# Optimization experiments

Hardware: AMD Instinct MI355X
Metric: run time of the kernel (lower is better)

The kernel has to match this reference:

```python
import jax, jax.numpy as jnp
import numpy as np

K = 3  # three_nn
EPS = 1e-10


def setup_inputs() -> dict:
    key = jax.random.key(0)
    ks = jax.random.split(key, 10)
    B, N, NP = 4, 16384, 4096
    C1, C2 = 128, 256
    Cin, H1, H2, Cout = C1 + C2, 256, 256, 128
    xyz1 = jax.random.normal(ks[0], (B, N, 3), dtype=jnp.float32)
    xyz2 = jax.random.normal(ks[1], (B, NP, 3), dtype=jnp.float32)
    features1 = jax.random.normal(ks[2], (B, N, C1), dtype=jnp.float32)
    features2 = jax.random.normal(ks[3], (B, NP, C2), dtype=jnp.float32)
    def lin(k, fan_in, fan_out):
        bound = 1.0 / np.sqrt(fan_in)
        kw, kb = jax.random.split(k)
        W = jax.random.uniform(kw, (fan_in, fan_out), jnp.float32, -bound, bound)
        b = jax.random.uniform(kb, (fan_out,), jnp.float32, -bound, bound)
        return W, b
    W1, b1 = lin(ks[4], Cin, H1)
    W2, b2 = lin(ks[5], H1, H2)
    W3, b3 = lin(ks[6], H2, Cout)
    return {"xyz1": xyz1, "xyz2": xyz2, "features1": features1,
            "features2": features2, "W1": W1, "b1": b1, "W2": W2,
            "b2": b2, "W3": W3, "b3": b3}


def _three_nn(xyz1, xyz2):
    # squared pairwise distances via |a|^2 + |b|^2 - 2 a.b  -> [B, N, npoint]
    sq1 = jnp.sum(xyz1 * xyz1, axis=-1)  # [B, N]
    sq2 = jnp.sum(xyz2 * xyz2, axis=-1)  # [B, npoint]
    dots = jnp.einsum("bnd,bmd->bnm", xyz1, xyz2)
    sqdist = sq1[:, :, None] + sq2[:, None, :] - 2.0 * dots
    neg_d, idx = jax.lax.top_k(-sqdist, K)  # 3 smallest squared distances
    return -neg_d, idx  # dist:[B,N,3], idx:[B,N,3]


def reference(xyz1, xyz2, features1, features2, W1, b1, W2, b2, W3, b3):
    B = xyz1.shape[0]
    dist, idx = _three_nn(xyz1, xyz2)
    # torch custom three_nn is non-differentiable in dist
    dist = jax.lax.stop_gradient(dist)
    dist = jnp.maximum(dist, EPS)
    recip = 1.0 / dist                                  # [B, N, 3]
    weight = recip / jnp.sum(recip, axis=-1, keepdims=True)
    # three_interpolate: gather neighbor features and weighted-sum
    batch_idx = jnp.arange(B)[:, None, None]
    gathered = features2[batch_idx, idx]                # [B, N, 3, C2]
    interp = jnp.einsum("bnkc,bnk->bnc", gathered, weight)
    new_features = jnp.concatenate([features1, interp], axis=-1)
    h = jax.nn.relu(new_features @ W1 + b1)
    h = jax.nn.relu(h @ W2 + b2)
    return h @ W3 + b3
```

## Files before the change

kernel.cpp:

```cpp
#include <hip/hip_runtime.h>
#include <stdint.h>

#define QT   65536
#define NPTS 4096
#define C1   128
#define C2   256
#define CIN  384
#define COUT 128

typedef _Float16 f16;
typedef __attribute__((ext_vector_type(8))) _Float16 f16x8;
typedef __attribute__((ext_vector_type(4))) float f32x4;

__device__ __attribute__((aligned(16))) f16 g_w1p[12 * 16 * 64 * 8];
__device__ __attribute__((aligned(16))) f16 g_w2p[8 * 16 * 64 * 8];
__device__ __attribute__((aligned(16))) f16 g_w3p[8 * 8 * 64 * 8];
__device__ __attribute__((aligned(16))) float4 g_cand[4 * NPTS];

__device__ inline void packW4(const float* __restrict__ W, f16* __restrict__ dst,
                              int i, int N, int NCB) {
  const int g = i & 3, quad = (i >> 2) & 3, cbk = i >> 4;
  const int cb = cbk % NCB, kcb = cbk / NCB;
  const int col = cb * 16 + g * 4;
  const int k0 = kcb * 32 + quad * 8;
  f16x8 o[4];
#pragma unroll
  for (int e = 0; e < 8; ++e) {
    float4 v = *(const float4*)(W + (size_t)(k0 + e) * N + col);
    o[0][e] = (f16)v.x; o[1][e] = (f16)v.y; o[2][e] = (f16)v.z; o[3][e] = (f16)v.w;
  }
  f16* base = dst + ((size_t)cbk * 64 + quad * 16 + g * 4) * 8;
#pragma unroll
  for (int j = 0; j < 4; ++j) *(f16x8*)(base + j * 8) = o[j];
}

__global__ __launch_bounds__(256) void prep(
    const float* __restrict__ xyz2, const float* __restrict__ W1,
    const float* __restrict__ W2,   const float* __restrict__ W3) {
  const int tid = blockIdx.x * 256 + threadIdx.x;
  const int nthr = gridDim.x * 256;
  for (int i = tid; i < 4 * NPTS; i += nthr) {
    const float* p = xyz2 + (size_t)i * 3;
    float x = p[0], y = p[1], z = p[2];
    g_cand[i] = make_float4(x, y, z, fmaf(x, x, fmaf(y, y, z * z)));
  }
  for (int i = tid; i < 12 * 16 * 16; i += nthr) packW4(W1, g_w1p, i, 256, 16);
  for (int i = tid; i < 8 * 16 * 16; i += nthr) packW4(W2, g_w2p, i, 256, 16);
  for (int i = tid; i < 8 * 8 * 16; i += nthr) packW4(W3, g_w3p, i, 128, 8);
}

__device__ inline uint32_t umin(uint32_t a, uint32_t b) { return a < b ? a : b; }
__device__ inline uint32_t med3u(uint32_t a, uint32_t b, uint32_t c) {
  uint32_t d;
  asm("v_med3_u32 %0, %1, %2, %3" : "=v"(d) : "v"(a), "v"(b), "v"(c));
  return d;
}

#define XS_STRIDE 392
#define HS_STRIDE 264
#define WV_OFF 50176
#define IV_OFF 51200
#define SMEM_BYTES 52224

__global__ __launch_bounds__(512) void fused_fp(
    const float* __restrict__ xyz1, const float* __restrict__ xyz2,
    const float* __restrict__ f1,   const float* __restrict__ f2,
    const float* __restrict__ W1,   const float* __restrict__ b1,
    const float* __restrict__ W2,   const float* __restrict__ b2,
    const float* __restrict__ W3,   const float* __restrict__ b3,
    float* __restrict__ out)
{
  __shared__ __align__(16) char smem[SMEM_BYTES];
  uint32_t* mgU  = (uint32_t*)(smem + 16384);
  float*    wvp  = (float*)(smem + WV_OFF);
  int*      ivp  = (int*)(smem + IV_OFF);
  f16*      Xs   = (f16*)smem;
  f16*      Hs   = (f16*)smem;

  const int t = threadIdx.x;
  const int r = t & 63;
  const int w = t >> 6;
  const int qb = blockIdx.x * 64;
  const int batch = qb >> 14;
  const float* xz2b = xyz2 + (size_t)batch * NPTS * 3;
  const float* f2b  = f2   + (size_t)batch * NPTS * C2;

  const int q = qb + r;
  const float qx = xyz1[q * 3], qy = xyz1[q * 3 + 1], qz = xyz1[q * 3 + 2];
  const float nx = -2.f * qx, ny = -2.f * qy, nz = -2.f * qz;
  const float sq1q = qx * qx + qy * qy + qz * qz;

  uint32_t k0 = ~0u, k1 = ~0u, k2 = ~0u, k3 = ~0u, k4 = ~0u;

  auto ins5 = [&](uint32_t c) {
    uint32_t n0 = umin(k0, c);
    uint32_t n1 = med3u(k0, k1, c);
    uint32_t n2 = med3u(k1, k2, c);
    uint32_t n3 = med3u(k2, k3, c);
    uint32_t n4 = med3u(k3, k4, c);
    k0 = n0; k1 = n1; k2 = n2; k3 = n3; k4 = n4;
  };
  auto packk = [&](float e, uint32_t idx) -> uint32_t {
    e = fmaxf(e, 0.f);
    return (__builtin_bit_cast(uint32_t, e) & 0xFFFFF000u) | idx;
  };

  {
    const int wu = __builtin_amdgcn_readfirstlane(w);
    const float4* __restrict__ cp = g_cand + (batch << 12) + (wu << 9);
    const uint32_t abase = (uint32_t)(wu << 9);
    #pragma unroll 2
    for (int m = 0; m < 512; m += 4) {
      float4 c0 = cp[m], c1 = cp[m + 1], c2 = cp[m + 2], c3 = cp[m + 3];
      float e0 = fmaf(nx, c0.x, fmaf(ny, c0.y, fmaf(nz, c0.z, c0.w))) + sq1q;
      float e1 = fmaf(nx, c1.x, fmaf(ny, c1.y, fmaf(nz, c1.z, c1.w))) + sq1q;
      float e2 = fmaf(nx, c2.x, fmaf(ny, c2.y, fmaf(nz, c2.z, c2.w))) + sq1q;
      float e3 = fmaf(nx, c3.x, fmaf(ny, c3.y, fmaf(nz, c3.z, c3.w))) + sq1q;
      ins5(packk(e0, abase + m));
      ins5(packk(e1, abase + m + 1));
      ins5(packk(e2, abase + m + 2));
      ins5(packk(e3, abase + m + 3));
    }
  }

  if (w > 0) {
    int base = ((w - 1) * 64 + r) * 5;
    mgU[base]     = k0;
    mgU[base + 1] = k1;
    mgU[base + 2] = k2;
    mgU[base + 3] = k3;
    mgU[base + 4] = k4;
  }
  __syncthreads();

  if (w == 0) {
    const double x1 = (double)qx, y1 = (double)qy, z1 = (double)qz;
    const double sq1 = x1 * x1 + y1 * y1 + z1 * z1;
    double d0 = 1e300, d1 = 1e300, d2 = 1e300;
    int j0 = 0, j1 = 0, j2 = 0;
    uint32_t surv[40];
    surv[0] = k0; surv[1] = k1; surv[2] = k2; surv[3] = k3; surv[4] = k4;
    #pragma unroll
    for (int wi = 0; wi < 7; ++wi)
      #pragma unroll
      for (int s = 0; s < 5; ++s)
        surv[5 + wi * 5 + s] = mgU[(wi * 64 + r) * 5 + s];
    #pragma unroll
    for (int s = 0; s < 40; ++s) {
      int idx = (int)(surv[s] & (NPTS - 1));
      const float* p2 = xz2b + (size_t)idx * 3;
      double x2 = (double)p2[0], y2 = (double)p2[1], z2 = (double)p2[2];
      double d = sq1 + (x2 * x2 + y2 * y2 + z2 * z2)
                     - 2.0 * (x1 * x2 + y1 * y2 + z1 * z2);
      bool c2 = (d < d2) || (d == d2 && idx < j2);
      bool c1 = (d < d1) || (d == d1 && idx < j1);
      bool c0 = (d < d0) || (d == d0 && idx < j0);
      d2 = c1 ? d1 : (c2 ? d : d2);  j2 = c1 ? j1 : (c2 ? idx : j2);
      d1 = c0 ? d0 : (c1 ? d : d1);  j1 = c0 ? j0 : (c1 ? idx : j1);
      d0 = c0 ? d : d0;              j0 = c0 ? idx : j0;
    }
    float e0 = fmaxf((float)d0, 1e-10f);
    float e1 = fmaxf((float)d1, 1e-10f);
    float e2 = fmaxf((float)d2, 1e-10f);
    float r0 = 1.f / e0, r1 = 1.f / e1, r2 = 1.f / e2;
    float inv = 1.f / (r0 + r1 + r2);
    wvp[r * 4 + 0] = r0 * inv; wvp[r * 4 + 1] = r1 * inv;
    wvp[r * 4 + 2] = r2 * inv; wvp[r * 4 + 3] = 0.f;
    ivp[r * 4 + 0] = j0; ivp[r * 4 + 1] = j1; ivp[r * 4 + 2] = j2; ivp[r * 4 + 3] = 0;
  }
  __syncthreads();

  {
    const int row = t >> 3, c = t & 7;
    f16* xr = Xs + row * XS_STRIDE;
    {
      const float* f1r = f1 + (size_t)(qb + row) * C1 + c * 16;
      float4 u0 = *(const float4*)(f1r);
      float4 u1 = *(const float4*)(f1r + 4);
      float4 u2 = *(const float4*)(f1r + 8);
      float4 u3 = *(const float4*)(f1r + 12);
      f16x8 o0, o1;
      o0[0] = (f16)u0.x; o0[1] = (f16)u0.y; o0[2] = (f16)u0.z; o0[3] = (f16)u0.w;
      o0[4] = (f16)u1.x; o0[5] = (f16)u1.y; o0[6] = (f16)u1.z; o0[7] = (f16)u1.w;
      o1[0] = (f16)u2.x; o1[1] = (f16)u2.y; o1[2] = (f16)u2.z; o1[3] = (f16)u2.w;
      o1[4] = (f16)u3.x; o1[5] = (f16)u3.y; o1[6] = (f16)u3.z; o1[7] = (f16)u3.w;
      *(f16x8*)(xr + c * 16)     = o0;
      *(f16x8*)(xr + c * 16 + 8) = o1;
    }
    const float w0 = wvp[row * 4 + 0], w1 = wvp[row * 4 + 1], w2 = wvp[row * 4 + 2];
    const float* p0 = f2b + (size_t)(ivp[row * 4 + 0] & (NPTS - 1)) * C2;
    const float* p1 = f2b + (size_t)(ivp[row * 4 + 1] & (NPTS - 1)) * C2;
    const float* p2 = f2b + (size_t)(ivp[row * 4 + 2] & (NPTS - 1)) * C2;
    #pragma unroll
    for (int ch = 0; ch < 4; ++ch) {
      const int col = ch * 64 + c * 8;
      float4 a0 = *(const float4*)(p0 + col), b0 = *(const float4*)(p0 + col + 4);
      float4 a1 = *(const float4*)(p1 + col), b1v = *(const float4*)(p1 + col + 4);
      float4 a2 = *(const float4*)(p2 + col), b2v = *(const float4*)(p2 + col + 4);
      f16x8 o;
      o[0] = (f16)(w0 * a0.x + w1 * a1.x + w2 * a2.x);
      o[1] = (f16)(w0 * a0.y + w1 * a1.y + w2 * a2.y);
      o[2] = (f16)(w0 * a0.z + w1 * a1.z + w2 * a2.z);
      o[3] = (f16)(w0 * a0.w + w1 * a1.w + w2 * a2.w);
      o[4] = (f16)(w0 * b0.x + w1 * b1v.x + w2 * b2v.x);
      o[5] = (f16)(w0 * b0.y + w1 * b1v.y + w2 * b2v.y);
      o[6] = (f16)(w0 * b0.z + w1 * b1v.z + w2 * b2v.z);
      o[7] = (f16)(w0 * b0.w + w1 * b1v.w + w2 * b2v.w);
      *(f16x8*)(xr + C1 + col) = o;
    }
  }
  __syncthreads();

  const int l16 = r & 15, quad = r >> 4;
  const int nb = w * 32;

  f32x4 acc[4][2];
  #pragma unroll
  for (int i = 0; i < 4; ++i)
    #pragma unroll
    for (int j = 0; j < 2; ++j) acc[i][j] = f32x4{0.f, 0.f, 0.f, 0.f};

  #pragma unroll
  for (int kc = 0; kc < CIN; kc += 32) {
    f16x8 a[4];
    #pragma unroll
    for (int i = 0; i < 4; ++i)
      a[i] = *(const f16x8*)(Xs + (i * 16 + l16) * XS_STRIDE + kc + quad * 8);
    f16x8 b[2];
    #pragma unroll
    for (int j = 0; j < 2; ++j)
      b[j] = *((const f16x8*)g_w1p +
               (size_t)((kc >> 5) * 16 + (w * 2 + j)) * 64 + r);
    #pragma unroll
    for (int i = 0; i < 4; ++i)
      #pragma unroll
      for (int j = 0; j < 2; ++j)
        acc[i][j] = __builtin_amdgcn_mfma_f32_16x16x32_f16(a[i], b[j], acc[i][j], 0, 0, 0);
  }
  __syncthreads();
  #pragma unroll
  for (int j = 0; j < 2; ++j) {
    float bv = b1[nb + j * 16 + l16];
    #pragma unroll
    for (int i = 0; i < 4; ++i)
      #pragma unroll
      for (int e = 0; e < 4; ++e) {
        int row = i * 16 + quad * 4 + e;
        Hs[row * HS_STRIDE + nb + j * 16 + l16] =
            (f16)fmaxf(acc[i][j][e] + bv, 0.f);
      }
  }
  __syncthreads();

  f32x4 acc2[4][2];
  #pragma unroll
  for (int i = 0; i < 4; ++i)
    #pragma unroll
    for (int j = 0; j < 2; ++j) acc2[i][j] = f32x4{0.f, 0.f, 0.f, 0.f};

  #pragma unroll
  for (int kc = 0; kc < 256; kc += 32) {
    f16x8 a[4];
    #pragma unroll
    for (int i = 0; i < 4; ++i)
      a[i] = *(const f16x8*)(Hs + (i * 16 + l16) * HS_STRIDE + kc + quad * 8);
    f16x8 b[2];
    #pragma unroll
    for (int j = 0; j < 2; ++j)
      b[j] = *((const f16x8*)g_w2p +
               (size_t)((kc >> 5) * 16 + (w * 2 + j)) * 64 + r);
    #pragma unroll
    for (int i = 0; i < 4; ++i)
      #pragma unroll
      for (int j = 0; j < 2; ++j)
        acc2[i][j] = __builtin_amdgcn_mfma_f32_16x16x32_f16(a[i], b[j], acc2[i][j], 0, 0, 0);
  }
  __syncthreads();
  #pragma unroll
  for (int j = 0; j < 2; ++j) {
    float bv = b2[nb + j * 16 + l16];
    #pragma unroll
    for (int i = 0; i < 4; ++i)
      #pragma unroll
      for (int e = 0; e < 4; ++e) {
        int row = i * 16 + quad * 4 + e;
        Hs[row * HS_STRIDE + nb + j * 16 + l16] =
            (f16)fmaxf(acc2[i][j][e] + bv, 0.f);
      }
  }
  __syncthreads();

  const int nb3 = w * 16;
  f32x4 acc3[4];
  #pragma unroll
  for (int i = 0; i < 4; ++i) acc3[i] = f32x4{0.f, 0.f, 0.f, 0.f};

  #pragma unroll
  for (int kc = 0; kc < 256; kc += 32) {
    f16x8 a[4];
    #pragma unroll
    for (int i = 0; i < 4; ++i)
      a[i] = *(const f16x8*)(Hs + (i * 16 + l16) * HS_STRIDE + kc + quad * 8);
    f16x8 b;
    b = *((const f16x8*)g_w3p + (size_t)((kc >> 5) * 8 + w) * 64 + r);
    #pragma unroll
    for (int i = 0; i < 4; ++i)
      acc3[i] = __builtin_amdgcn_mfma_f32_16x16x32_f16(a[i], b, acc3[i], 0, 0, 0);
  }
  {
    int col = nb3 + l16;
    float bv = b3[col];
    #pragma unroll
    for (int i = 0; i < 4; ++i)
      #pragma unroll
      for (int e = 0; e < 4; ++e) {
        int row = i * 16 + quad * 4 + e;
        out[(size_t)(qb + row) * COUT + col] = acc3[i][e] + bv;
      }
  }
}

extern "C" void kernel_launch(void* const* d_in, const int* in_sizes, int n_in,
                              void* d_out, int out_size, void* d_ws, size_t ws_size,
                              hipStream_t stream)
{
  (void)out_size; (void)d_ws; (void)ws_size;
  static const int expect[10] = {196608, 49152, 8388608, 4194304,
                                 98304, 256, 65536, 256, 32768, 128};
  const void* p[10];
  bool ok = (n_in == 10);
  if (ok) {
    bool used[10] = {false};
    for (int e = 0; e < 10; ++e) {
      p[e] = nullptr;
      for (int i = 0; i < 10; ++i) {
        if (!used[i] && in_sizes[i] == expect[e]) {
          p[e] = d_in[i]; used[i] = true; break;
        }
      }
      if (!p[e]) { ok = false; break; }
    }
  }
  if (!ok)
    for (int e = 0; e < 10; ++e) p[e] = d_in[e < n_in ? e : (n_in - 1)];

  prep<<<256, 256, 0, stream>>>(
      (const float*)p[1], (const float*)p[4],
      (const float*)p[6], (const float*)p[8]);

  fused_fp<<<QT / 64, 512, 0, stream>>>(
      (const float*)p[0], (const float*)p[1],
      (const float*)p[2], (const float*)p[3],
      (const float*)p[4], (const float*)p[5],
      (const float*)p[6], (const float*)p[7],
      (const float*)p[8], (const float*)p[9],
      (float*)d_out);
}
```

Baseline: 225.9 us.

## Parallelize double-precision neighbor refinement across all waves before merging

Each of the 8 waves now rescores its own 5 surviving candidates in double precision and writes its top 3 (distance and index) to shared memory. Wave 0 then only merges 24 precomputed entries instead of rescoring 40 candidates with scattered global loads. A bias of 0.05 is added to the packed float key so it stays positive, which lets the clamp be dropped. This spreads the serial fp64 work across waves but adds shared-memory traffic for doubles, and the biased truncated keys could change which candidates survive.

```diff
diff --git a/kernel.cpp b/kernel.cpp
--- a/kernel.cpp
+++ b/kernel.cpp
@@ -58,6 +58,8 @@
 
 #define XS_STRIDE 392
 #define HS_STRIDE 264
+#define DMPD_OFF 16384
+#define DMPI_OFF 28672
 #define WV_OFF 50176
 #define IV_OFF 51200
 #define SMEM_BYTES 52224
@@ -71,7 +73,8 @@
     float* __restrict__ out)
 {
   __shared__ __align__(16) char smem[SMEM_BYTES];
-  uint32_t* mgU  = (uint32_t*)(smem + 16384);
+  double*   dmpD = (double*)(smem + DMPD_OFF);
+  int*      dmpI = (int*)(smem + DMPI_OFF);
   float*    wvp  = (float*)(smem + WV_OFF);
   int*      ivp  = (int*)(smem + IV_OFF);
   f16*      Xs   = (f16*)smem;
@@ -101,7 +104,6 @@
     k0 = n0; k1 = n1; k2 = n2; k3 = n3; k4 = n4;
   };
   auto packk = [&](float e, uint32_t idx) -> uint32_t {
-    e = fmaxf(e, 0.f);
     return (__builtin_bit_cast(uint32_t, e) & 0xFFFFF000u) | idx;
   };
 
@@ -109,13 +111,14 @@
     const int wu = __builtin_amdgcn_readfirstlane(w);
     const float4* __restrict__ cp = g_cand + (batch << 12) + (wu << 9);
     const uint32_t abase = (uint32_t)(wu << 9);
+    const float sbias = sq1q + 0.05f;
     #pragma unroll 2
     for (int m = 0; m < 512; m += 4) {
       float4 c0 = cp[m], c1 = cp[m + 1], c2 = cp[m + 2], c3 = cp[m + 3];
-      float e0 = fmaf(nx, c0.x, fmaf(ny, c0.y, fmaf(nz, c0.z, c0.w))) + sq1q;
-      float e1 = fmaf(nx, c1.x, fmaf(ny, c1.y, fmaf(nz, c1.z, c1.w))) + sq1q;
-      float e2 = fmaf(nx, c2.x, fmaf(ny, c2.y, fmaf(nz, c2.z, c2.w))) + sq1q;
-      float e3 = fmaf(nx, c3.x, fmaf(ny, c3.y, fmaf(nz, c3.z, c3.w))) + sq1q;
+      float e0 = fmaf(nx, c0.x, fmaf(ny, c0.y, fmaf(nz, c0.z, c0.w))) + sbias;
+      float e1 = fmaf(nx, c1.x, fmaf(ny, c1.y, fmaf(nz, c1.z, c1.w))) + sbias;
+      float e2 = fmaf(nx, c2.x, fmaf(ny, c2.y, fmaf(nz, c2.z, c2.w))) + sbias;
+      float e3 = fmaf(nx, c3.x, fmaf(ny, c3.y, fmaf(nz, c3.z, c3.w))) + sbias;
       ins5(packk(e0, abase + m));
       ins5(packk(e1, abase + m + 1));
       ins5(packk(e2, abase + m + 2));
@@ -123,31 +126,15 @@
     }
   }
 
-  if (w > 0) {
-    int base = ((w - 1) * 64 + r) * 5;
-    mgU[base]     = k0;
-    mgU[base + 1] = k1;
-    mgU[base + 2] = k2;
-    mgU[base + 3] = k3;
-    mgU[base + 4] = k4;
-  }
-  __syncthreads();
-
-  if (w == 0) {
+  {
     const double x1 = (double)qx, y1 = (double)qy, z1 = (double)qz;
     const double sq1 = x1 * x1 + y1 * y1 + z1 * z1;
     double d0 = 1e300, d1 = 1e300, d2 = 1e300;
     int j0 = 0, j1 = 0, j2 = 0;
-    uint32_t surv[40];
-    surv[0] = k0; surv[1] = k1; surv[2] = k2; surv[3] = k3; surv[4] = k4;
-    #pragma unroll
-    for (int wi = 0; wi < 7; ++wi)
-      #pragma unroll
-      for (int s = 0; s < 5; ++s)
-        surv[5 + wi * 5 + s] = mgU[(wi * 64 + r) * 5 + s];
-    #pragma unroll
-    for (int s = 0; s < 40; ++s) {
-      int idx = (int)(surv[s] & (NPTS - 1));
+    uint32_t sv[5] = {k0, k1, k2, k3, k4};
+    #pragma unroll
+    for (int s = 0; s < 5; ++s) {
+      int idx = (int)(sv[s] & (NPTS - 1));
       const float* p2 = xz2b + (size_t)idx * 3;
       double x2 = (double)p2[0], y2 = (double)p2[1], z2 = (double)p2[2];
       double d = sq1 + (x2 * x2 + y2 * y2 + z2 * z2)
@@ -158,6 +145,31 @@
       d2 = c1 ? d1 : (c2 ? d : d2);  j2 = c1 ? j1 : (c2 ? idx : j2);
       d1 = c0 ? d0 : (c1 ? d : d1);  j1 = c0 ? j0 : (c1 ? idx : j1);
       d0 = c0 ? d : d0;              j0 = c0 ? idx : j0;
+    }
+    const int base = (w * 64 + r) * 3;
+    dmpD[base]     = d0;  dmpI[base]     = j0;
+    dmpD[base + 1] = d1;  dmpI[base + 1] = j1;
+    dmpD[base + 2] = d2;  dmpI[base + 2] = j2;
+  }
+  __syncthreads();
+
+  if (w == 0) {
+    double d0 = 1e300, d1 = 1e300, d2 = 1e300;
+    int j0 = 0, j1 = 0, j2 = 0;
+    #pragma unroll
+    for (int w2 = 0; w2 < 8; ++w2) {
+      #pragma unroll
+      for (int s = 0; s < 3; ++s) {
+        const int base = (w2 * 64 + r) * 3 + s;
+        double d = dmpD[base];
+        int idx  = dmpI[base];
+        bool c2 = (d < d2) || (d == d2 && idx < j2);
+        bool c1 = (d < d1) || (d == d1 && idx < j1);
+        bool c0 = (d < d0) || (d == d0 && idx < j0);
+        d2 = c1 ? d1 : (c2 ? d : d2);  j2 = c1 ? j1 : (c2 ? idx : j2);
+        d1 = c0 ? d0 : (c1 ? d : d1);  j1 = c0 ? j0 : (c1 ? idx : j1);
+        d0 = c0 ? d : d0;              j0 = c0 ? idx : j0;
+      }
     }
     float e0 = fmaxf((float)d0, 1e-10f);
     float e1 = fmaxf((float)d1, 1e-10f);
```

Result: faster. 215.0 us (-4.8%).
